# Optimization experiments

Hardware: AMD Instinct MI355X
Metric: run time of the kernel (lower is better)

## Reference

```python
import jax, jax.numpy as jnp
import numpy as np

DIM = 1024
HEADS = 16
SCALE = DIM ** -0.5  # NOTE: original uses full dim, not head dim


def setup_inputs() -> dict:
    key = jax.random.key(0)
    k1, k2, k3, k4 = jax.random.split(key, 4)
    x = jax.random.normal(k1, (2, 2048, DIM), dtype=jnp.float32)
    # torch nn.Linear(dim, 3*dim, bias=False): y = x @ W_qkv (stored here as [dim, 3*dim])
    w_qkv = jax.random.normal(k2, (DIM, 3 * DIM), dtype=jnp.float32) * (DIM ** -0.5)
    w_out = jax.random.normal(k3, (DIM, DIM), dtype=jnp.float32) * (DIM ** -0.5)
    b_out = jax.random.normal(k4, (DIM,), dtype=jnp.float32) * 0.01
    return {"x": x, "w_qkv": w_qkv, "w_out": w_out, "b_out": b_out}


def reference(x, w_qkv, w_out, b_out):
    b, n, d = x.shape
    h = HEADS
    hd = d // h
    qkv = x @ w_qkv  # [b, n, 3*d]
    # last dim layout is (qkv, h, hd) per rearrange 'b n (qkv h d) -> qkv b h n d'
    qkv = qkv.reshape(b, n, 3, h, hd)
    q, k, v = (jnp.moveaxis(qkv, (2, 3), (0, 2))[i] for i in range(3))  # each [b, h, n, hd]
    dots = jnp.einsum('bhid,bhjd->bhij', q, k) * SCALE
    causal_mask = jnp.triu(jnp.ones((n, n), dtype=bool), k=1)
    dots = jnp.where(causal_mask, -jnp.inf, dots)
    attn = jax.nn.softmax(dots, axis=-1)
    out = jnp.einsum('bhij,bhjd->bhid', attn, v)
    out = jnp.moveaxis(out, 1, 2).reshape(b, n, d)  # 'b h n d -> b n (h d)'
    return out @ w_out + b_out
```

## Files before the change

### kernel.cpp

```cpp
#include <hip/hip_runtime.h>

typedef __attribute__((ext_vector_type(8))) short bf16x8;
typedef __attribute__((ext_vector_type(4))) float f32x4;
typedef unsigned short u16;
typedef unsigned int u32;

#define SEQ 2048
#define NHEAD 16
#define EXP2_SCALE 0.045084219f

__device__ __forceinline__ u16 f2bf(float f){
  u32 u = __builtin_bit_cast(u32, f);
  u += 0x7FFFu + ((u >> 16) & 1u);
  return (u16)(u >> 16);
}

__device__ __forceinline__ void gl16(const u16* g, u16* l){
  __builtin_amdgcn_global_load_lds(
      (__attribute__((address_space(1))) void*)(unsigned long long)(const void*)g,
      (__attribute__((address_space(3))) void*)(unsigned)(unsigned long long)(const void*)l,
      16, 0, 0);
}

__global__ __launch_bounds__(256) void prep(const float* __restrict__ x,
                                            const float* __restrict__ w_qkv,
                                            const float* __restrict__ w_out,
                                            u16* __restrict__ xb,
                                            u16* __restrict__ wqkvT,
                                            u16* __restrict__ woutT){
  __shared__ u16 t[32][33];
  const int bid = blockIdx.x;
  if (bid < 4096){
    int i = (bid * 256 + threadIdx.x) << 2;
    float4 v = *(const float4*)&x[i];
    ushort4 o;
    o.x = f2bf(v.x); o.y = f2bf(v.y); o.z = f2bf(v.z); o.w = f2bf(v.w);
    *(ushort4*)&xb[i] = o;
    return;
  }
  const float* src; u16* dst; int R, C, bx, by;
  if (bid < 7168){ int tt = bid - 4096; src = w_qkv; dst = wqkvT; R = 1024; C = 3072; bx = tt % 96; by = tt / 96; }
  else           { int tt = bid - 7168; src = w_out; dst = woutT; R = 1024; C = 1024; bx = tt % 32; by = tt / 32; }
  const int c0 = bx << 5, r0 = by << 5;
  const int tx = threadIdx.x & 31, tg = threadIdx.x >> 5;
  #pragma unroll
  for (int i = 0; i < 4; i++){
    int r = (tg << 2) + i;
    t[r][tx] = f2bf(src[(size_t)(r0 + r) * C + (c0 + tx)]);
  }
  __syncthreads();
  #pragma unroll
  for (int i = 0; i < 4; i++){
    int c = (tg << 2) + i;
    dst[(size_t)(c0 + c) * R + (r0 + tx)] = t[tx][c];
  }
}

__global__ __launch_bounds__(256) void gemm_qkv(const u16* __restrict__ A,
                                                const u16* __restrict__ Bt,
                                                u16* __restrict__ Qo,
                                                u16* __restrict__ Ko,
                                                u16* __restrict__ Vto){
  __shared__ u16 As[128 * 64];
  __shared__ u16 Bs[128 * 64];
  const int tid = threadIdx.x;
  const int lane = tid & 63, wid = tid >> 6;
  const int l15 = lane & 15, quad = lane >> 4;
  const int wm = wid >> 1, wn = wid & 1;
  const int bm = blockIdx.y << 7, bn = blockIdx.x << 7;
  const int qkv_idx = bn >> 10;

  const int lr = lane >> 3;
  const int cc = (lane & 7) ^ lr;
  const u16* gA0 = A  + (size_t)(bm + wid * 32 + lr) * 1024 + (cc << 3);
  const u16* gB0 = Bt + (size_t)(bn + wid * 32 + lr) * 1024 + (cc << 3);
  u16* lA0 = &As[wid * 2048];
  u16* lB0 = &Bs[wid * 2048];

  f32x4 acc[4][4];
  #pragma unroll
  for (int i = 0; i < 4; i++)
    #pragma unroll
    for (int j = 0; j < 4; j++) acc[i][j] = (f32x4){0.f, 0.f, 0.f, 0.f};

  const bool vbranch = (qkv_idx == 2);
  for (int k0 = 0; k0 < 1024; k0 += 64){
    #pragma unroll
    for (int t = 0; t < 4; t++){
      gl16(gA0 + k0 + t * 8192, lA0 + t * 512);
      gl16(gB0 + k0 + t * 8192, lB0 + t * 512);
    }
    __syncthreads();
    #pragma unroll
    for (int hf = 0; hf < 2; hf++){
      bf16x8 af[4], bfr[4];
      #pragma unroll
      for (int mt = 0; mt < 4; mt++){
        int row = wm * 64 + mt * 16 + l15;
        af[mt] = *(const bf16x8*)&As[row * 64 + (((hf * 4 + quad) ^ (row & 7)) << 3)];
      }
      #pragma unroll
      for (int nt = 0; nt < 4; nt++){
        int row = wn * 64 + nt * 16 + l15;
        bfr[nt] = *(const bf16x8*)&Bs[row * 64 + (((hf * 4 + quad) ^ (row & 7)) << 3)];
      }
      if (!vbranch){
        #pragma unroll
        for (int mt = 0; mt < 4; mt++)
          #pragma unroll
          for (int nt = 0; nt < 4; nt++)
            acc[mt][nt] = __builtin_amdgcn_mfma_f32_16x16x32_bf16(af[mt], bfr[nt], acc[mt][nt], 0, 0, 0);
      } else {
        #pragma unroll
        for (int mt = 0; mt < 4; mt++)
          #pragma unroll
          for (int nt = 0; nt < 4; nt++)
            acc[mt][nt] = __builtin_amdgcn_mfma_f32_16x16x32_bf16(bfr[nt], af[mt], acc[mt][nt], 0, 0, 0);
      }
    }
    __syncthreads();
  }

  if (!vbranch){
    const float qscale = (qkv_idx == 0) ? EXP2_SCALE : 1.0f;
    #pragma unroll
    for (int mt = 0; mt < 4; mt++){
      #pragma unroll
      for (int nt = 0; nt < 4; nt++){
        int col = bn + wn * 64 + nt * 16 + l15;
        int head = (col & 1023) >> 6, hd_i = col & 63;
        #pragma unroll
        for (int r = 0; r < 4; r++){
          int row = bm + wm * 64 + mt * 16 + quad * 4 + r;
          int b = row >> 11, pos = row & 2047;
          size_t bh = ((size_t)(b * NHEAD + head)) << 17;
          u16 v = f2bf(acc[mt][nt][r] * qscale);
          if (qkv_idx == 0) Qo[bh + ((size_t)pos << 6) + hd_i] = v;
          else              Ko[bh + ((size_t)pos << 6) + hd_i] = v;
        }
      }
    }
  } else {
    #pragma unroll
    for (int mt = 0; mt < 4; mt++){
      int row_m = bm + wm * 64 + mt * 16 + l15;
      int b = row_m >> 11, pos = row_m & 2047;
      #pragma unroll
      for (int nt = 0; nt < 4; nt++){
        #pragma unroll
        for (int r = 0; r < 4; r++){
          int c = bn + wn * 64 + nt * 16 + quad * 4 + r;
          int head = (c & 1023) >> 6, hd_i = c & 63;
          size_t bh = ((size_t)(b * NHEAD + head)) << 17;
          Vto[bh + ((size_t)hd_i << 11) + pos] = f2bf(acc[mt][nt][r]);
        }
      }
    }
  }
}

__global__ __launch_bounds__(256) void attn_kernel(const u16* __restrict__ Q,
                                                   const u16* __restrict__ K,
                                                   const u16* __restrict__ Vt,
                                                   u16* __restrict__ Oo){
  __shared__ u16 Ks[128 * 64];
  __shared__ u16 Vts[64 * 128];
  __shared__ u16 Ps[4][16 * 136];
  const int tid = threadIdx.x;
  const int lane = tid & 63, wid = tid >> 6;
  const int l15 = lane & 15, quad = lane >> 4;
  const int bh = blockIdx.x & 31;
  const int qt2 = 15 - (blockIdx.x >> 5);
  const size_t base = ((size_t)bh) << 17;
  const int b = bh >> 4, h = bh & 15;

  const u16* qsrc = Q + base + ((size_t)((qt2 << 7) + wid * 16 + l15) << 6) + quad * 8;
  bf16x8 bq[2][2];
  bq[0][0] = *(const bf16x8*)qsrc;
  bq[0][1] = *(const bf16x8*)(qsrc + 32);
  bq[1][0] = *(const bf16x8*)(qsrc + 4096);
  bq[1][1] = *(const bf16x8*)(qsrc + 4096 + 32);

  const int rK = wid * 32 + (lane >> 3);
  const int cK = (lane & 7) ^ (rK & 7);
  const u16* gK0 = K + base + ((size_t)rK << 6) + (cK << 3);
  u16* lK = &Ks[wid * 2048];
  const u16* gV[4];
  #pragma unroll
  for (int t = 0; t < 4; t++){
    int rv = wid * 16 + t * 4 + (lane >> 4);
    int cv = (lane & 15) ^ (rv & 15);
    gV[t] = Vt + base + (size_t)rv * 2048 + (cv << 3);
  }
  u16* lV = &Vts[wid * 2048];

  f32x4 o[8];
  #pragma unroll
  for (int i = 0; i < 8; i++) o[i] = (f32x4){0.f, 0.f, 0.f, 0.f};
  float lsum[2] = {0.f, 0.f};
  const int qp0 = (qt2 << 7) + wid * 16 + l15;
  const int jt_max = qt2;
  u16* Pw = &Ps[wid][0];

  for (int jt = 0; jt <= jt_max; jt++){
    const u16* gk = gK0 + (size_t)jt * 8192;
    #pragma unroll
    for (int t = 0; t < 4; t++) gl16(gk + t * 512, lK + t * 512);
    #pragma unroll
    for (int t = 0; t < 4; t++) gl16(gV[t] + (jt << 7), lV + t * 512);
    __syncthreads();

    const bool diag = (jt == jt_max);
    #pragma unroll
    for (int s = 0; s < 2; s++){
      f32x4 st[8];
      #pragma unroll
      for (int mt = 0; mt < 8; mt++) st[mt] = (f32x4){0.f, 0.f, 0.f, 0.f};
      #pragma unroll
      for (int mt = 0; mt < 8; mt++){
        int kvr = mt * 16 + l15;
        bf16x8 ak0 = *(const bf16x8*)&Ks[kvr * 64 + ((quad ^ (kvr & 7)) << 3)];
        st[mt] = __builtin_amdgcn_mfma_f32_16x16x32_bf16(ak0, bq[s][0], st[mt], 0, 0, 0);
        bf16x8 ak1 = *(const bf16x8*)&Ks[kvr * 64 + (((4 + quad) ^ (kvr & 7)) << 3)];
        st[mt] = __builtin_amdgcn_mfma_f32_16x16x32_bf16(ak1, bq[s][1], st[mt], 0, 0, 0);
      }

      const int qpos = qp0 + s * 64;
      float rs = 0.f;
      #pragma unroll
      for (int mt = 0; mt < 8; mt++){
        float pr[4];
        #pragma unroll
        for (int r = 0; r < 4; r++){
          float w = st[mt][r];
          if (diag){
            int kv = (jt << 7) + mt * 16 + quad * 4 + r;
            if (kv > qpos) w = -INFINITY;
          }
          pr[r] = __builtin_amdgcn_exp2f(w);
        }
        rs += (pr[0] + pr[1]) + (pr[2] + pr[3]);
        u32 a0 = __builtin_bit_cast(u32, pr[0]) + 0x8000u;
        u32 a1 = __builtin_bit_cast(u32, pr[1]) + 0x8000u;
        u32 a2 = __builtin_bit_cast(u32, pr[2]) + 0x8000u;
        u32 a3 = __builtin_bit_cast(u32, pr[3]) + 0x8000u;
        uint2 pk;
        pk.x = __builtin_amdgcn_perm(a1, a0, 0x07060302u);
        pk.y = __builtin_amdgcn_perm(a3, a2, 0x07060302u);
        *(uint2*)&Pw[l15 * 136 + mt * 16 + quad * 4] = pk;
      }
      rs += __shfl_xor(rs, 16);
      rs += __shfl_xor(rs, 32);
      lsum[s] += rs;

      #pragma unroll
      for (int ks = 0; ks < 4; ks++){
        bf16x8 bp = *(const bf16x8*)&Pw[l15 * 136 + ks * 32 + quad * 8];
        #pragma unroll
        for (int dt = 0; dt < 4; dt++){
          int dr = dt * 16 + l15;
          bf16x8 av = *(const bf16x8*)&Vts[dr * 128 + (((ks * 4 + quad) ^ (dr & 15)) << 3)];
          o[s * 4 + dt] = __builtin_amdgcn_mfma_f32_16x16x32_bf16(av, bp, o[s * 4 + dt], 0, 0, 0);
        }
      }
    }
    __syncthreads();
  }

  #pragma unroll
  for (int s = 0; s < 2; s++){
    float inv = 1.f / lsum[s];
    const size_t orow = (size_t)((b << 11) + qp0 + s * 64) * 1024 + h * 64;
    #pragma unroll
    for (int dt = 0; dt < 4; dt++){
      ushort4 w;
      w.x = f2bf(o[s * 4 + dt][0] * inv); w.y = f2bf(o[s * 4 + dt][1] * inv);
      w.z = f2bf(o[s * 4 + dt][2] * inv); w.w = f2bf(o[s * 4 + dt][3] * inv);
      *(ushort4*)&Oo[orow + dt * 16 + quad * 4] = w;
    }
  }
}

__global__ __launch_bounds__(256) void gemm_out(const u16* __restrict__ A,
                                                const u16* __restrict__ Bt,
                                                const float* __restrict__ bias,
                                                float* __restrict__ out){
  __shared__ u16 As[128 * 64];
  __shared__ u16 Bs[128 * 64];
  const int tid = threadIdx.x;
  const int lane = tid & 63, wid = tid >> 6;
  const int l15 = lane & 15, quad = lane >> 4;
  const int wm = wid >> 1, wn = wid & 1;
  const int bm = blockIdx.y << 7, bn = blockIdx.x << 7;

  const int lr = lane >> 3;
  const int cc = (lane & 7) ^ lr;
  const u16* gA0 = A  + (size_t)(bm + wid * 32 + lr) * 1024 + (cc << 3);
  const u16* gB0 = Bt + (size_t)(bn + wid * 32 + lr) * 1024 + (cc << 3);
  u16* lA0 = &As[wid * 2048];
  u16* lB0 = &Bs[wid * 2048];

  f32x4 acc[4][4];
  #pragma unroll
  for (int i = 0; i < 4; i++)
    #pragma unroll
    for (int j = 0; j < 4; j++) acc[i][j] = (f32x4){0.f, 0.f, 0.f, 0.f};

  for (int k0 = 0; k0 < 1024; k0 += 64){
    #pragma unroll
    for (int t = 0; t < 4; t++){
      gl16(gA0 + k0 + t * 8192, lA0 + t * 512);
      gl16(gB0 + k0 + t * 8192, lB0 + t * 512);
    }
    __syncthreads();
    #pragma unroll
    for (int hf = 0; hf < 2; hf++){
      bf16x8 af[4], bfr[4];
      #pragma unroll
      for (int mt = 0; mt < 4; mt++){
        int row = wm * 64 + mt * 16 + l15;
        af[mt] = *(const bf16x8*)&As[row * 64 + (((hf * 4 + quad) ^ (row & 7)) << 3)];
      }
      #pragma unroll
      for (int nt = 0; nt < 4; nt++){
        int row = wn * 64 + nt * 16 + l15;
        bfr[nt] = *(const bf16x8*)&Bs[row * 64 + (((hf * 4 + quad) ^ (row & 7)) << 3)];
      }
      #pragma unroll
      for (int mt = 0; mt < 4; mt++)
        #pragma unroll
        for (int nt = 0; nt < 4; nt++)
          acc[mt][nt] = __builtin_amdgcn_mfma_f32_16x16x32_bf16(af[mt], bfr[nt], acc[mt][nt], 0, 0, 0);
    }
    __syncthreads();
  }

  #pragma unroll
  for (int nt = 0; nt < 4; nt++){
    int col = bn + wn * 64 + nt * 16 + l15;
    float bv = bias[col];
    #pragma unroll
    for (int mt = 0; mt < 4; mt++)
      #pragma unroll
      for (int r = 0; r < 4; r++){
        int row = bm + wm * 64 + mt * 16 + quad * 4 + r;
        out[(size_t)row * 1024 + col] = acc[mt][nt][r] + bv;
      }
  }
}

extern "C" void kernel_launch(void* const* d_in, const int* in_sizes, int n_in,
                              void* d_out, int out_size, void* d_ws, size_t ws_size,
                              hipStream_t stream){
  const float* x     = (const float*)d_in[0];
  const float* w_qkv = (const float*)d_in[1];
  const float* w_out = (const float*)d_in[2];
  const float* b_out = (const float*)d_in[3];
  float* out = (float*)d_out;

  char* ws = (char*)d_ws;
  u16* xb    = (u16*)(ws);
  u16* wqkvT = (u16*)(ws + (8u  << 20));
  u16* woutT = (u16*)(ws + (14u << 20));
  u16* Qb    = (u16*)(ws + (16u << 20));
  u16* Kb    = (u16*)(ws + (24u << 20));
  u16* Vtb   = (u16*)(ws + (32u << 20));
  u16* attn  = (u16*)(ws + (40u << 20));

  prep<<<8192, 256, 0, stream>>>(x, w_qkv, w_out, xb, wqkvT, woutT);
  gemm_qkv<<<dim3(24, 32), 256, 0, stream>>>(xb, wqkvT, Qb, Kb, Vtb);
  attn_kernel<<<dim3(512), 256, 0, stream>>>(Qb, Kb, Vtb, attn);
  gemm_out<<<dim3(8, 32), 256, 0, stream>>>(attn, woutT, b_out, out);
}
```

Measured before the change: 202.3 us.

## Halve attention query tile to 64 rows and double grid size

Each attention block now handles 64 query rows instead of 128, with each wave owning one 16-row slice, and the grid doubles to 1024 blocks. The goal is more parallelism and occupancy, a finer causal tail that skips wasted work for the lower query half, and fewer registers from dropping the second accumulator set. In exchange, every K/V tile is loaded from global memory twice as often across blocks, which raises load traffic and barrier count per unit of work. The diagonal-masking branch is also split out so that only the last iteration runs the mask.

```diff
diff --git a/kernel.cpp b/kernel.cpp
--- a/kernel.cpp
+++ b/kernel.cpp
@@ -170,16 +170,13 @@
   const int lane = tid & 63, wid = tid >> 6;
   const int l15 = lane & 15, quad = lane >> 4;
   const int bh = blockIdx.x & 31;
-  const int qt2 = 15 - (blockIdx.x >> 5);
+  const int qt = 31 - (blockIdx.x >> 5);
   const size_t base = ((size_t)bh) << 17;
   const int b = bh >> 4, h = bh & 15;
 
-  const u16* qsrc = Q + base + ((size_t)((qt2 << 7) + wid * 16 + l15) << 6) + quad * 8;
-  bf16x8 bq[2][2];
-  bq[0][0] = *(const bf16x8*)qsrc;
-  bq[0][1] = *(const bf16x8*)(qsrc + 32);
-  bq[1][0] = *(const bf16x8*)(qsrc + 4096);
-  bq[1][1] = *(const bf16x8*)(qsrc + 4096 + 32);
+  const u16* qsrc = Q + base + ((size_t)((qt << 6) + wid * 16 + l15) << 6) + quad * 8;
+  const bf16x8 bq0 = *(const bf16x8*)qsrc;
+  const bf16x8 bq1 = *(const bf16x8*)(qsrc + 32);
 
   const int rK = wid * 32 + (lane >> 3);
   const int cK = (lane & 7) ^ (rK & 7);
@@ -194,15 +191,15 @@
   }
   u16* lV = &Vts[wid * 2048];
 
-  f32x4 o[8];
-  #pragma unroll
-  for (int i = 0; i < 8; i++) o[i] = (f32x4){0.f, 0.f, 0.f, 0.f};
-  float lsum[2] = {0.f, 0.f};
-  const int qp0 = (qt2 << 7) + wid * 16 + l15;
-  const int jt_max = qt2;
+  f32x4 o[4];
+  #pragma unroll
+  for (int dt = 0; dt < 4; dt++) o[dt] = (f32x4){0.f, 0.f, 0.f, 0.f};
+  float lsum = 0.f;
+  const int qpos = (qt << 6) + wid * 16 + l15;
+  const int jt_max = qt >> 1;
   u16* Pw = &Ps[wid][0];
 
-  for (int jt = 0; jt <= jt_max; jt++){
+  auto kv_iter = [&](const int jt, const bool diag) __attribute__((always_inline)) {
     const u16* gk = gK0 + (size_t)jt * 8192;
     #pragma unroll
     for (int t = 0; t < 4; t++) gl16(gk + t * 512, lK + t * 512);
@@ -210,74 +207,67 @@
     for (int t = 0; t < 4; t++) gl16(gV[t] + (jt << 7), lV + t * 512);
     __syncthreads();
 
-    const bool diag = (jt == jt_max);
-    #pragma unroll
-    for (int s = 0; s < 2; s++){
-      f32x4 st[8];
-      #pragma unroll
-      for (int mt = 0; mt < 8; mt++) st[mt] = (f32x4){0.f, 0.f, 0.f, 0.f};
-      #pragma unroll
-      for (int mt = 0; mt < 8; mt++){
-        int kvr = mt * 16 + l15;
-        bf16x8 ak0 = *(const bf16x8*)&Ks[kvr * 64 + ((quad ^ (kvr & 7)) << 3)];
-        st[mt] = __builtin_amdgcn_mfma_f32_16x16x32_bf16(ak0, bq[s][0], st[mt], 0, 0, 0);
-        bf16x8 ak1 = *(const bf16x8*)&Ks[kvr * 64 + (((4 + quad) ^ (kvr & 7)) << 3)];
-        st[mt] = __builtin_amdgcn_mfma_f32_16x16x32_bf16(ak1, bq[s][1], st[mt], 0, 0, 0);
-      }
-
-      const int qpos = qp0 + s * 64;
-      float rs = 0.f;
-      #pragma unroll
-      for (int mt = 0; mt < 8; mt++){
-        float pr[4];
-        #pragma unroll
-        for (int r = 0; r < 4; r++){
-          float w = st[mt][r];
-          if (diag){
-            int kv = (jt << 7) + mt * 16 + quad * 4 + r;
-            if (kv > qpos) w = -INFINITY;
-          }
-          pr[r] = __builtin_amdgcn_exp2f(w);
+    f32x4 st[8];
+    #pragma unroll
+    for (int mt = 0; mt < 8; mt++) st[mt] = (f32x4){0.f, 0.f, 0.f, 0.f};
+    #pragma unroll
+    for (int mt = 0; mt < 8; mt++){
+      int kvr = mt * 16 + l15;
+      bf16x8 ak0 = *(const bf16x8*)&Ks[kvr * 64 + ((quad ^ (kvr & 7)) << 3)];
+      st[mt] = __builtin_amdgcn_mfma_f32_16x16x32_bf16(ak0, bq0, st[mt], 0, 0, 0);
+      bf16x8 ak1 = *(const bf16x8*)&Ks[kvr * 64 + (((4 + quad) ^ (kvr & 7)) << 3)];
+      st[mt] = __builtin_amdgcn_mfma_f32_16x16x32_bf16(ak1, bq1, st[mt], 0, 0, 0);
+    }
+
+    #pragma unroll
+    for (int mt = 0; mt < 8; mt++){
+      float pr[4];
+      #pragma unroll
+      for (int r = 0; r < 4; r++){
+        float w = st[mt][r];
+        if (diag){
+          int kv = (jt << 7) + mt * 16 + quad * 4 + r;
+          if (kv > qpos) w = -INFINITY;
         }
-        rs += (pr[0] + pr[1]) + (pr[2] + pr[3]);
-        u32 a0 = __builtin_bit_cast(u32, pr[0]) + 0x8000u;
-        u32 a1 = __builtin_bit_cast(u32, pr[1]) + 0x8000u;
-        u32 a2 = __builtin_bit_cast(u32, pr[2]) + 0x8000u;
-        u32 a3 = __builtin_bit_cast(u32, pr[3]) + 0x8000u;
-        uint2 pk;
-        pk.x = __builtin_amdgcn_perm(a1, a0, 0x07060302u);
-        pk.y = __builtin_amdgcn_perm(a3, a2, 0x07060302u);
-        *(uint2*)&Pw[l15 * 136 + mt * 16 + quad * 4] = pk;
-      }
-      rs += __shfl_xor(rs, 16);
-      rs += __shfl_xor(rs, 32);
-      lsum[s] += rs;
-
-      #pragma unroll
-      for (int ks = 0; ks < 4; ks++){
-        bf16x8 bp = *(const bf16x8*)&Pw[l15 * 136 + ks * 32 + quad * 8];
-        #pragma unroll
-        for (int dt = 0; dt < 4; dt++){
-          int dr = dt * 16 + l15;
-          bf16x8 av = *(const bf16x8*)&Vts[dr * 128 + (((ks * 4 + quad) ^ (dr & 15)) << 3)];
-          o[s * 4 + dt] = __builtin_amdgcn_mfma_f32_16x16x32_bf16(av, bp, o[s * 4 + dt], 0, 0, 0);
-        }
-      }
-    }
-    __syncthreads();
-  }
-
-  #pragma unroll
-  for (int s = 0; s < 2; s++){
-    float inv = 1.f / lsum[s];
-    const size_t orow = (size_t)((b << 11) + qp0 + s * 64) * 1024 + h * 64;
-    #pragma unroll
-    for (int dt = 0; dt < 4; dt++){
-      ushort4 w;
-      w.x = f2bf(o[s * 4 + dt][0] * inv); w.y = f2bf(o[s * 4 + dt][1] * inv);
-      w.z = f2bf(o[s * 4 + dt][2] * inv); w.w = f2bf(o[s * 4 + dt][3] * inv);
-      *(ushort4*)&Oo[orow + dt * 16 + quad * 4] = w;
-    }
+        pr[r] = __builtin_amdgcn_exp2f(w);
+      }
+      lsum += (pr[0] + pr[1]) + (pr[2] + pr[3]);
+      u32 a0 = __builtin_bit_cast(u32, pr[0]) + 0x8000u;
+      u32 a1 = __builtin_bit_cast(u32, pr[1]) + 0x8000u;
+      u32 a2 = __builtin_bit_cast(u32, pr[2]) + 0x8000u;
+      u32 a3 = __builtin_bit_cast(u32, pr[3]) + 0x8000u;
+      uint2 pk;
+      pk.x = __builtin_amdgcn_perm(a1, a0, 0x07060302u);
+      pk.y = __builtin_amdgcn_perm(a3, a2, 0x07060302u);
+      *(uint2*)&Pw[l15 * 136 + mt * 16 + quad * 4] = pk;
+    }
+
+    #pragma unroll
+    for (int ks = 0; ks < 4; ks++){
+      bf16x8 bp = *(const bf16x8*)&Pw[l15 * 136 + ks * 32 + quad * 8];
+      #pragma unroll
+      for (int dt = 0; dt < 4; dt++){
+        int dr = dt * 16 + l15;
+        bf16x8 av = *(const bf16x8*)&Vts[dr * 128 + (((ks * 4 + quad) ^ (dr & 15)) << 3)];
+        o[dt] = __builtin_amdgcn_mfma_f32_16x16x32_bf16(av, bp, o[dt], 0, 0, 0);
+      }
+    }
+    __syncthreads();
+  };
+
+  for (int jt = 0; jt < jt_max; jt++) kv_iter(jt, false);
+  kv_iter(jt_max, true);
+
+  lsum += __shfl_xor(lsum, 16);
+  lsum += __shfl_xor(lsum, 32);
+  float inv = 1.f / lsum;
+  const size_t orow = (size_t)((b << 11) + qpos) * 1024 + h * 64;
+  #pragma unroll
+  for (int dt = 0; dt < 4; dt++){
+    ushort4 w;
+    w.x = f2bf(o[dt][0] * inv); w.y = f2bf(o[dt][1] * inv);
+    w.z = f2bf(o[dt][2] * inv); w.w = f2bf(o[dt][3] * inv);
+    *(ushort4*)&Oo[orow + dt * 16 + quad * 4] = w;
   }
 }
 
@@ -369,6 +359,6 @@
 
   prep<<<8192, 256, 0, stream>>>(x, w_qkv, w_out, xb, wqkvT, woutT);
   gemm_qkv<<<dim3(24, 32), 256, 0, stream>>>(xb, wqkvT, Qb, Kb, Vtb);
-  attn_kernel<<<dim3(512), 256, 0, stream>>>(Qb, Kb, Vtb, attn);
+  attn_kernel<<<dim3(1024), 256, 0, stream>>>(Qb, Kb, Vtb, attn);
   gemm_out<<<dim3(8, 32), 256, 0, stream>>>(attn, woutT, b_out, out);
 }
```

After: 175.8 us. 1.15x faster.
